# Kernel optimization log

Hardware: AMD Instinct MI355X
Metric: run time of the kernel (lower is better)

The kernel has to match this reference:

```python
import jax, jax.numpy as jnp
import numpy as np

N = 100000; E = 1600000
X_DIM = 128; Y_DIM = 32; H_DIM = 128; R_DIM = 128; Z_DIM = 64
TAU = 1.0; KEEP = 0.1  # dropout p=0.9 -> keep prob 0.1


def spmm(edge_index, edge_weight, h):
    # out[row] += w * h[col]  (sparse [N,N] @ dense [N,D])
    row, col = edge_index[0], edge_index[1]
    return jax.ops.segment_sum(h[col] * edge_weight[:, None], row, num_segments=N)


def setup_inputs() -> dict:
    key = jax.random.key(0)
    ks = jax.random.split(key, 32)
    p = lambda k, shp: (0.02 * jax.random.normal(k, shp)).astype(jnp.float32)
    inp = {
        'x': jax.random.normal(ks[0], (N, X_DIM), dtype=jnp.float32),
        'y_': jax.random.uniform(ks[1], (N, Y_DIM), dtype=jnp.float32),
        'edge_index': jax.random.randint(ks[2], (2, E), 0, N, dtype=jnp.int32),
        'edge_weight': jax.random.uniform(ks[3], (E,), dtype=jnp.float32),
        'non_label': jax.random.bernoulli(ks[4], 0.5, (N,)),
        # inverted dropout mask, torch semantics: keep w.p. 0.1, scale by 1/0.1
        'dropout_mask': (jax.random.bernoulli(ks[5], KEEP, (N, X_DIM)).astype(jnp.float32) / KEEP),
        'u_gumbel': jax.random.uniform(ks[6], (N, Y_DIM), dtype=jnp.float32),
        'z_eps': jax.random.normal(ks[7], (Z_DIM,), dtype=jnp.float32),
        # x_to_yu (2-layer spmm GCN)
        'Wg1': p(ks[8], (X_DIM, H_DIM)), 'bg1': jnp.zeros((H_DIM,), jnp.float32),
        'Wg2': p(ks[9], (H_DIM, Y_DIM)), 'bg2': jnp.zeros((Y_DIM,), jnp.float32),
        # GSNN_Encoder
        'W_xy': p(ks[10], (H_DIM + Y_DIM, R_DIM)), 'b_xy': jnp.zeros((R_DIM,), jnp.float32),
        'W_hr': p(ks[11], (R_DIM, R_DIM)), 'b_hr': jnp.zeros((R_DIM,), jnp.float32),
        # R_to_MuSigma
        'W_rh': p(ks[12], (R_DIM, R_DIM)), 'b_rh': jnp.zeros((R_DIM,), jnp.float32),
        'W_mu': p(ks[13], (R_DIM, Z_DIM)), 'b_mu': jnp.zeros((Z_DIM,), jnp.float32),
        'W_sig': p(ks[14], (R_DIM, Z_DIM)), 'b_sig': jnp.zeros((Z_DIM,), jnp.float32),
        # GSNN_Decoder
        'W_xh': p(ks[15], (X_DIM, H_DIM)), 'b_xh': jnp.zeros((H_DIM,), jnp.float32),
        'W_h2': p(ks[16], (H_DIM + Z_DIM, H_DIM + Z_DIM)), 'b_h2': jnp.zeros((H_DIM + Z_DIM,), jnp.float32),
        'W_hy': p(ks[17], (H_DIM + Z_DIM, Y_DIM)), 'b_hy': jnp.zeros((Y_DIM,), jnp.float32),
    }
    return inp


def reference(x, y_, edge_index, edge_weight, non_label, dropout_mask, u_gumbel, z_eps,
              Wg1, bg1, Wg2, bg2, W_xy, b_xy, W_hr, b_hr,
              W_rh, b_rh, W_mu, b_mu, W_sig, b_sig,
              W_xh, b_xh, W_h2, b_h2, W_hy, b_hy):
    # ---- x_to_yu: 2-layer spmm GCN -> (y_encode [N,Y], y_embedding [N,H]) ----
    h_emb = jax.nn.relu(spmm(edge_index, edge_weight, x) @ Wg1 + bg1)
    y_encode = spmm(edge_index, edge_weight, h_emb) @ Wg2 + bg2
    # ---- gumbel_softmax(hard=True, tau=1) at non-labelled nodes ----
    g = -jnp.log(-jnp.log(u_gumbel + 1e-10) + 1e-10)
    soft = jax.nn.softmax((y_encode + g) / TAU, axis=-1)
    hard = jax.nn.one_hot(jnp.argmax(soft, axis=-1), Y_DIM, dtype=soft.dtype)
    y_gumbel = hard + soft - jax.lax.stop_gradient(soft)  # straight-through
    y = jnp.where(non_label[:, None], y_gumbel, y_)
    # ---- GSNN_Encoder (adj unused, matching original) ----
    h_enc = jax.nn.relu(jnp.concatenate([h_emb, y], axis=1) @ W_xy + b_xy)
    r_nodes = h_enc @ W_hr + b_hr
    r_graph = jnp.mean(r_nodes, axis=0)  # readout [R]
    # ---- R_to_MuSigma + rsample ----
    hr = jax.nn.relu(r_graph @ W_rh + b_rh)
    mu = hr @ W_mu + b_mu
    sigma = 0.1 + 0.9 * jax.nn.sigmoid(hr @ W_sig + b_sig)
    z = mu + sigma * z_eps  # Normal.rsample
    # ---- GSNN_Decoder ----
    xd = x * dropout_mask
    h = jax.nn.relu(xd @ W_xh + b_xh)
    h = jnp.concatenate([h, jnp.broadcast_to(z, (h.shape[0], Z_DIM))], axis=1)
    h = h / (jnp.linalg.norm(h, axis=1, keepdims=True) + 1e-06)
    h = jax.nn.relu(spmm(edge_index, edge_weight, h) @ W_h2 + b_h2)
    y_pred = spmm(edge_index, edge_weight, h) @ W_hy + b_hy
    return y_pred
```

## Files before the change

### kernel.cpp

```cpp
#include <hip/hip_runtime.h>
#include <hip/hip_bf16.h>

#define NN 100000
#define EE 1600000

typedef unsigned short u16;
typedef unsigned int   u32;
typedef short short8 __attribute__((ext_vector_type(8)));
typedef float v4f    __attribute__((ext_vector_type(4)));
typedef u32 u32x2    __attribute__((ext_vector_type(2)));

__device__ __forceinline__ float b2f(u16 h){ u32 u = ((u32)h) << 16; return __builtin_bit_cast(float, u); }
__device__ __forceinline__ float lo2f(u32 u){ return __builtin_bit_cast(float, u << 16); }
__device__ __forceinline__ float hi2f(u32 u){ return __builtin_bit_cast(float, u & 0xffff0000u); }
__device__ __forceinline__ u16   f2b(float f){ __hip_bfloat16 h = __float2bfloat16(f); return __builtin_bit_cast(u16, h); }
__device__ __forceinline__ float ldx(const void* p, long i, int fm){
  return fm ? ((const float*)p)[i] : b2f(((const u16*)p)[i]);
}
__device__ __forceinline__ float i2f(int v){ return __builtin_bit_cast(float, v); }

__global__ void k_detect(const void* __restrict__ x, const void* __restrict__ nonlab,
                         int* __restrict__ flags){
  __shared__ int s_bad, s_ni, s_nf, s_nb;
  int t = threadIdx.x;
  if (t == 0){ s_bad = 0; s_ni = 0; s_nf = 0; s_nb = 0; }
  __syncthreads();
  u32 w = ((const u32*)x)[t];
  u32 lo = w & 0xffffu, ex = (lo >> 7) & 0xffu;
  if (lo != 0u && (ex < 100u || ex > 140u)) atomicAdd(&s_bad, 1);
  if (t < 64){
    u32 v = ((const u32*)nonlab)[t];
    if (v > 1u) atomicAdd(&s_ni, 1);
    if (v != 0u && v != 0x3F800000u) atomicAdd(&s_nf, 1);
  }
  if (t < 128){
    u16 h = ((const u16*)nonlab)[t];
    if (h != 0 && h != 0x3F80) atomicAdd(&s_nb, 1);
  }
  __syncthreads();
  if (t == 0){
    flags[0] = (s_bad > 32) ? 1 : 0;
    flags[1] = (s_ni == 0) ? 1 : ((s_nf == 0) ? 3 : ((s_nb == 0) ? 2 : 0));
  }
}

#define PW_G1 0
#define PW_G2 16384
#define PW_XY 20480
#define PW_XH 40960
#define PW_H2 57344
#define PW_HY 94208
#define PW_TOT 100352
#define PB_G1 0
#define PB_XY 128
#define PB_XH 256
#define PB_H2 384
#define PB_ZERO 576
#define PB_HY 704
#define PB_TOT 736

__global__ __launch_bounds__(256) void k_pack(const void* W0, const void* W1, const void* W2,
                      const void* W3, const void* W4, const void* W5,
                      const void* b0, const void* b1, const void* b2, const void* b3, const void* b4,
                      u16* __restrict__ Wp, float* __restrict__ bp, const int* __restrict__ flags){
  int e = blockIdx.x * 256 + threadIdx.x;
  int fm = flags[0];
  if (e < PW_TOT){
    const void* src; int off, DOUT;
    if      (e < PW_G2){ src = W0; off = PW_G1; DOUT = 128; }
    else if (e < PW_XY){ src = W1; off = PW_G2; DOUT = 32; }
    else if (e < PW_XH){ src = W2; off = PW_XY; DOUT = 128; }
    else if (e < PW_H2){ src = W3; off = PW_XH; DOUT = 128; }
    else if (e < PW_HY){ src = W4; off = PW_H2; DOUT = 192; }
    else               { src = W5; off = PW_HY; DOUT = 32; }
    int local = e - off;
    int k = local / DOUT, col = local - k * DOUT;
    u16 v = fm ? f2b(((const float*)src)[local]) : ((const u16*)src)[local];
    Wp[off + ((k >> 3) * DOUT + col) * 8 + (k & 7)] = v;
  }
  int eb = e - PW_TOT;
  if (eb >= 0 && eb < PB_TOT){
    float v = 0.f;
    if      (eb < 128) v = ldx(b0, eb, fm);
    else if (eb < 256) v = ldx(b1, eb - 128, fm);
    else if (eb < 384) v = ldx(b2, eb - 256, fm);
    else if (eb < 576) v = ldx(b3, eb - 384, fm);
    else if (eb < 704) v = 0.f;
    else               v = ldx(b4, eb - 704, fm);
    bp[eb] = v;
  }
}

#define BSH 9
#define NBK 196
#define CAP 16384

__global__ __launch_bounds__(256) void k_front(const void* __restrict__ x,
     const u16* __restrict__ Wg1p, u16* __restrict__ xpo, const int* __restrict__ flags,
     const int* __restrict__ ei, const void* __restrict__ ew,
     int* __restrict__ bcnt, int2* __restrict__ stage){
  if (blockIdx.x < 1563){
    constexpr int STEPS = 4, CT = 4, RTW = 2, G = 2;
    int wid = blockIdx.x * 4 + (threadIdx.x >> 6);
    if (wid >= 6250) return;
    int g = wid % G; long chunk = wid / G;
    int lane = threadIdx.x & 63, n = lane & 15, q = lane >> 4;
    int colOff = g * 64;
    int fm = flags[0];
    short8 B[CT][STEPS];
    #pragma unroll
    for (int ct = 0; ct < CT; ++ct){
      int col = colOff + ct * 16 + n;
      #pragma unroll
      for (int s = 0; s < STEPS; ++s)
        B[ct][s] = *(const short8*)(Wg1p + (((s * 4 + q) * 128) + col) * 8);
    }
    for (int rt = 0; rt < RTW; ++rt){
      long rowbase = (chunk * RTW + rt) * 16;
      long arow = rowbase + n;
      v4f acc[CT] = {};
      #pragma unroll
      for (int s = 0; s < STEPS; ++s){
        short8 a;
        long base = arow * 128 + s * 32 + q * 8;
        if (fm){
          const float* xp = (const float*)x + base;
          float4 x0 = *(const float4*)xp, x1 = *(const float4*)(xp + 4);
          a[0] = (short)f2b(x0.x); a[1] = (short)f2b(x0.y);
          a[2] = (short)f2b(x0.z); a[3] = (short)f2b(x0.w);
          a[4] = (short)f2b(x1.x); a[5] = (short)f2b(x1.y);
          a[6] = (short)f2b(x1.z); a[7] = (short)f2b(x1.w);
        } else {
          a = *(const short8*)((const u16*)x + base);
        }
        #pragma unroll
        for (int ct = 0; ct < CT; ++ct)
          acc[ct] = __builtin_amdgcn_mfma_f32_16x16x32_bf16(a, B[ct][s], acc[ct], 0, 0, 0);
      }
      long orow = rowbase + q * 4;
      #pragma unroll
      for (int ct = 0; ct < CT; ++ct){
        int col = colOff + ct * 16 + n;
        #pragma unroll
        for (int r = 0; r < 4; ++r)
          xpo[(orow + r) * 128 + col] = f2b(acc[ct][r]);
      }
    }
  } else {
    __shared__ int lcnt[NBK];
    __shared__ int lbase[NBK];
    int t = threadIdx.x;
    int bid = blockIdx.x - 1563;
    for (int i = t; i < NBK; i += 256) lcnt[i] = 0;
    __syncthreads();
    int fm = flags[0];
    long e0 = (long)bid * 4096;
    int bb[16], ord[16], pk[16], wb[16];
    #pragma unroll
    for (int j = 0; j < 16; ++j){
      long e = e0 + j * 256 + t;
      bool v = e < EE;
      int r = v ? ei[e] : 0;
      int c = v ? ei[EE + e] : 0;
      float w = v ? ldx(ew, e, fm) : 0.f;
      int b = r >> BSH;
      bb[j] = v ? b : -1;
      pk[j] = ((r & 511) << 17) | c;
      wb[j] = __builtin_bit_cast(int, w);
      if (v) ord[j] = atomicAdd(&lcnt[b], 1);
    }
    __syncthreads();
    for (int i = t; i < NBK; i += 256){
      int c = lcnt[i];
      lbase[i] = c ? atomicAdd(&bcnt[i], c) : 0;
    }
    __syncthreads();
    #pragma unroll
    for (int j = 0; j < 16; ++j){
      if (bb[j] >= 0){
        int pos = lbase[bb[j]] + ord[j];
        if (pos < CAP) stage[(long)bb[j] * CAP + pos] = make_int2(pk[j], wb[j]);
      }
    }
  }
}

__global__ void k_scanB(const int* __restrict__ bcnt, int* __restrict__ bbase,
                        int* __restrict__ rowptr){
  __shared__ int l[256];
  int t = threadIdx.x;
  int v = (t < NBK) ? bcnt[t] : 0;
  l[t] = v; __syncthreads();
  for (int o = 1; o < 256; o <<= 1){
    int x = (t >= o) ? l[t - o] : 0; __syncthreads();
    l[t] += x; __syncthreads();
  }
  if (t < NBK) bbase[t] = l[t] - v;
  if (t == 0) rowptr[NN] = EE;
}

__global__ __launch_bounds__(512) void k_binB(const int* __restrict__ bbase, const int* __restrict__ bcnt,
                      const int2* __restrict__ stage, int2* __restrict__ cpk,
                      int* __restrict__ rowptr){
  __shared__ int cnt[512];
  __shared__ int cur[512];
  int b = blockIdx.x, t = threadIdx.x;
  int r0 = b << BSH;
  int rows = min(512, NN - r0);
  cnt[t] = 0; __syncthreads();
  int cb = min(bcnt[b], CAP);
  const int2* sb = stage + (long)b * CAP;
  for (int j = t; j < cb; j += 512)
    atomicAdd(&cnt[((u32)sb[j].x) >> 17], 1);
  __syncthreads();
  int v = cnt[t];
  cur[t] = v; __syncthreads();
  for (int o = 1; o < 512; o <<= 1){
    int x = (t >= o) ? cur[t - o] : 0; __syncthreads();
    cur[t] += x; __syncthreads();
  }
  int excl = bbase[b] + cur[t] - v;
  if (t < rows) rowptr[r0 + t] = excl;
  __syncthreads();
  cur[t] = excl;
  __syncthreads();
  for (int j = t; j < cb; j += 512){
    int2 w = sb[j];
    int rib = ((u32)w.x) >> 17;
    int pos = atomicAdd(&cur[rib], 1);
    cpk[pos] = make_int2(w.x & 0x1FFFF, w.y);
  }
}

template<bool AG, bool EPI>
__global__ __launch_bounds__(256) void k_spmm(const u16* __restrict__ in, u16* __restrict__ out,
                       const int* __restrict__ rowptr, const int2* __restrict__ cpk,
                       const float* __restrict__ agt, float* __restrict__ agg,
                       const float* __restrict__ bias){
  int wid  = blockIdx.x * 4 + (threadIdx.x >> 6);
  int lane = threadIdx.x & 63;
  if (wid >= NN) return;
  int half = lane >> 5, l16 = lane & 31;
  int s = rowptr[wid], e = rowptr[wid + 1];
  float a0 = 0.f, a1 = 0.f, a2 = 0.f, a3 = 0.f, aga = 0.f;
  for (int j = s; j < e; j += 8){
    int2 pe[4];
    if (j + 8 <= e){
      #pragma unroll
      for (int k = 0; k < 4; ++k) pe[k] = cpk[j + 2 * k + half];
    } else {
      #pragma unroll
      for (int k = 0; k < 4; ++k){
        int idx = j + 2 * k + half;
        int2 w = cpk[idx < e ? idx : j];
        if (idx >= e) w.y = 0;
        pe[k] = w;
      }
    }
    u32x2 u[4];
    #pragma unroll
    for (int k = 0; k < 4; ++k)
      u[k] = *(const u32x2*)(in + (long)pe[k].x * 128 + 4 * l16);
    if (AG && l16 == 0){
      #pragma unroll
      for (int k = 0; k < 4; ++k) aga = fmaf(i2f(pe[k].y), agt[pe[k].x], aga);
    }
    #pragma unroll
    for (int k = 0; k < 4; ++k){
      float wt = i2f(pe[k].y);
      a0 = fmaf(wt, lo2f(u[k].x), a0);
      a1 = fmaf(wt, hi2f(u[k].x), a1);
      a2 = fmaf(wt, lo2f(u[k].y), a2);
      a3 = fmaf(wt, hi2f(u[k].y), a3);
    }
  }
  a0 += __shfl_xor(a0, 32); a1 += __shfl_xor(a1, 32);
  a2 += __shfl_xor(a2, 32); a3 += __shfl_xor(a3, 32);
  if (AG) aga += __shfl_xor(aga, 32);
  if (EPI){
    a0 = fmaxf(a0 + bias[4 * l16],     0.f);
    a1 = fmaxf(a1 + bias[4 * l16 + 1], 0.f);
    a2 = fmaxf(a2 + bias[4 * l16 + 2], 0.f);
    a3 = fmaxf(a3 + bias[4 * l16 + 3], 0.f);
  }
  if (half == 0){
    u32x2 w;
    w.x = (u32)f2b(a0) | ((u32)f2b(a1) << 16);
    w.y = (u32)f2b(a2) | ((u32)f2b(a3) << 16);
    *(u32x2*)(out + (long)wid * 128 + 4 * l16) = w;
    if (AG && l16 == 0) agg[wid] = aga;
  }
}

__global__ __launch_bounds__(256) void k_spmm32b(const u16* __restrict__ in, void* __restrict__ out,
                       const int* __restrict__ rowptr, const int2* __restrict__ cpk,
                       const int* __restrict__ flags, const float* __restrict__ bp){
  int row = blockIdx.x * 16 + (threadIdx.x >> 4);
  int d = threadIdx.x & 15;
  if (row >= NN) return;
  int eh = d >> 3, d8 = d & 7;
  int fm = flags[0];
  int s = rowptr[row], e = rowptr[row + 1];
  float a0 = 0.f, a1 = 0.f, a2 = 0.f, a3 = 0.f;
  for (int j = s; j < e; j += 8){
    int2 p[4];
    if (j + 8 <= e){
      #pragma unroll
      for (int k = 0; k < 4; ++k) p[k] = cpk[j + 2 * k + eh];
    } else {
      #pragma unroll
      for (int k = 0; k < 4; ++k){
        int idx = j + 2 * k + eh;
        int2 w = cpk[idx < e ? idx : j];
        if (idx >= e) w.y = 0;
        p[k] = w;
      }
    }
    u32x2 u[4];
    #pragma unroll
    for (int k = 0; k < 4; ++k) u[k] = *(const u32x2*)(in + (long)p[k].x * 32 + 4 * d8);
    #pragma unroll
    for (int k = 0; k < 4; ++k){
      float wt = i2f(p[k].y);
      a0 = fmaf(wt, lo2f(u[k].x), a0);
      a1 = fmaf(wt, hi2f(u[k].x), a1);
      a2 = fmaf(wt, lo2f(u[k].y), a2);
      a3 = fmaf(wt, hi2f(u[k].y), a3);
    }
  }
  a0 += __shfl_xor(a0, 8); a1 += __shfl_xor(a1, 8);
  a2 += __shfl_xor(a2, 8); a3 += __shfl_xor(a3, 8);
  a0 += bp[4 * d8]; a1 += bp[4 * d8 + 1]; a2 += bp[4 * d8 + 2]; a3 += bp[4 * d8 + 3];
  if (eh == 0){
    if (fm){
      float4 w = make_float4(a0, a1, a2, a3);
      *(float4*)((float*)out + (long)row * 32 + 4 * d8) = w;
    } else {
      u32x2 w;
      w.x = (u32)f2b(a0) | ((u32)f2b(a1) << 16);
      w.y = (u32)f2b(a2) | ((u32)f2b(a3) << 16);
      *(u32x2*)((u16*)out + (long)row * 32 + 4 * d8) = w;
    }
  }
}

__global__ __launch_bounds__(256) void k_spmmg(const u16* __restrict__ in, u16* __restrict__ y,
                       const int* __restrict__ rowptr, const int2* __restrict__ cpk,
                       const int* __restrict__ flags, const void* __restrict__ bg2,
                       const void* __restrict__ ug, const void* __restrict__ ylab,
                       const void* __restrict__ nonlab){
  int row = blockIdx.x * 16 + (threadIdx.x >> 4);
  int d = threadIdx.x & 15;
  if (row >= NN) return;
  int fm = flags[0], mode = flags[1];
  bool nl;
  if      (mode == 1) nl = ((const int*)nonlab)[row] != 0;
  else if (mode == 3) nl = ((const float*)nonlab)[row] != 0.f;
  else if (mode == 2) nl = ((const u16*)nonlab)[row] != 0;
  else                nl = ((const unsigned char*)nonlab)[row] != 0;
  long base = (long)row * 32;
  if (!nl){
    u32 lo, hi;
    if (fm){
      lo = (u32)f2b(((const float*)ylab)[base + 2 * d]);
      hi = (u32)f2b(((const float*)ylab)[base + 2 * d + 1]);
    } else {
      lo = ((const u16*)ylab)[base + 2 * d];
      hi = ((const u16*)ylab)[base + 2 * d + 1];
    }
    *(u32*)(y + base + 2 * d) = lo | (hi << 16);
    return;
  }
  int eh = d >> 3, d8 = d & 7;
  int s = rowptr[row], e = rowptr[row + 1];
  float a0 = 0.f, a1 = 0.f, a2 = 0.f, a3 = 0.f;
  for (int j = s; j < e; j += 8){
    int2 p[4];
    if (j + 8 <= e){
      #pragma unroll
      for (int k = 0; k < 4; ++k) p[k] = cpk[j + 2 * k + eh];
    } else {
      #pragma unroll
      for (int k = 0; k < 4; ++k){
        int idx = j + 2 * k + eh;
        int2 w = cpk[idx < e ? idx : j];
        if (idx >= e) w.y = 0;
        p[k] = w;
      }
    }
    u32x2 u[4];
    #pragma unroll
    for (int k = 0; k < 4; ++k) u[k] = *(const u32x2*)(in + (long)p[k].x * 32 + 4 * d8);
    #pragma unroll
    for (int k = 0; k < 4; ++k){
      float wt = i2f(p[k].y);
      a0 = fmaf(wt, lo2f(u[k].x), a0);
      a1 = fmaf(wt, hi2f(u[k].x), a1);
      a2 = fmaf(wt, lo2f(u[k].y), a2);
      a3 = fmaf(wt, hi2f(u[k].y), a3);
    }
  }
  a0 += __shfl_xor(a0, 8); a1 += __shfl_xor(a1, 8);
  a2 += __shfl_xor(a2, 8); a3 += __shfl_xor(a3, 8);
  float av[4] = {a0, a1, a2, a3};
  int c0 = 4 * d8;
  float bm = -1e30f; int bi = 0;
  #pragma unroll
  for (int jj = 0; jj < 4; ++jj){
    float uu = ldx(ug, base + c0 + jj, fm);
    float g = -logf(-logf(uu + 1e-10f) + 1e-10f);
    float v = av[jj] + ldx(bg2, c0 + jj, fm) + g;
    if (v > bm){ bm = v; bi = c0 + jj; }
  }
  #pragma unroll
  for (int o = 1; o < 16; o <<= 1){
    float om = __shfl_xor(bm, o);
    int   oi = __shfl_xor(bi, o);
    if (om > bm || (om == bm && oi < bi)){ bm = om; bi = oi; }
  }
  if (eh == 0){
    u32x2 w;
    w.x = ((c0     == bi) ? 0x3F80u : 0u) | (((c0 + 1 == bi) ? 0x3F80u : 0u) << 16);
    w.y = ((c0 + 2 == bi) ? 0x3F80u : 0u) | (((c0 + 3 == bi) ? 0x3F80u : 0u) << 16);
    *(u32x2*)(y + base + c0) = w;
  }
}

template<int K, int DOUT, int CT, int RTW, bool RELU, int AMODE, int OMODE, bool CSUM>
__global__ __launch_bounds__(256) void k_mm(const u16* __restrict__ A, const void* __restrict__ A2,
     const void* __restrict__ A3, const u16* __restrict__ Wp, const float* __restrict__ bp,
     void* __restrict__ outv, const int* __restrict__ flags, float* __restrict__ csacc){
  constexpr int STEPS = K / 32;
  constexpr int G = DOUT / (16 * CT);
  constexpr int CHUNKS = 6250 / RTW;
  __shared__ float lsum[128];
  int wid = blockIdx.x * 4 + (threadIdx.x >> 6);
  if (wid >= G * CHUNKS) return;
  int g = wid % G; long chunk = wid / G;
  int lane = threadIdx.x & 63, n = lane & 15, q = lane >> 4;
  int colOff = g * CT * 16;

  if (CSUM){
    if (threadIdx.x < 128) lsum[threadIdx.x] = 0.f;
    __syncthreads();
  }

  short8 B[CT][STEPS];
  float bv[CT];
  #pragma unroll
  for (int ct = 0; ct < CT; ++ct){
    int col = colOff + ct * 16 + n;
    bv[ct] = bp[col];
    #pragma unroll
    for (int s = 0; s < STEPS; ++s)
      B[ct][s] = *(const short8*)(Wp + (((s * 4 + q) * DOUT) + col) * 8);
  }

  float csum[CT];
  #pragma unroll
  for (int ct = 0; ct < CT; ++ct) csum[ct] = 0.f;

  for (int rt = 0; rt < RTW; ++rt){
    long rowbase = (chunk * RTW + rt) * 16;
    long arow = rowbase + n;
    v4f acc[CT] = {};
    #pragma unroll
    for (int s = 0; s < STEPS; ++s){
      short8 a;
      if (AMODE == 0){
        a = *(const short8*)(A + arow * K + s * 32 + q * 8);
      } else {
        if (s < 4) a = *(const short8*)(A + arow * 128 + s * 32 + q * 8);
        else       a = *(const short8*)((const u16*)A2 + arow * 32 + q * 8);
      }
      #pragma unroll
      for (int ct = 0; ct < CT; ++ct)
        acc[ct] = __builtin_amdgcn_mfma_f32_16x16x32_bf16(a, B[ct][s], acc[ct], 0, 0, 0);
    }
    long orow = rowbase + q * 4;
    #pragma unroll
    for (int ct = 0; ct < CT; ++ct){
      int col = colOff + ct * 16 + n;
      #pragma unroll
      for (int r = 0; r < 4; ++r){
        float v = acc[ct][r] + bv[ct];
        if (RELU) v = fmaxf(v, 0.f);
        if (CSUM) csum[ct] += v;
        if (OMODE != 3){
          long oi = (orow + r) * (long)DOUT + col;
          ((u16*)outv)[oi] = f2b(v);
        }
      }
    }
  }
  if (CSUM){
    #pragma unroll
    for (int ct = 0; ct < CT; ++ct){
      csum[ct] += __shfl_xor(csum[ct], 16);
      csum[ct] += __shfl_xor(csum[ct], 32);
      if (lane < 16) atomicAdd(&lsum[colOff + ct * 16 + n], csum[ct]);
    }
    __syncthreads();
    if (threadIdx.x < 128) csacc[(long)blockIdx.x * 128 + threadIdx.x] = lsum[threadIdx.x];
  }
}

__global__ __launch_bounds__(256) void k_mmh2(const u16* __restrict__ A, const float* __restrict__ AG2,
     const float* __restrict__ zbuf, const u16* __restrict__ Wh2p, const float* __restrict__ bh2p,
     const u16* __restrict__ Whyp, u16* __restrict__ tbuf){
  __shared__ u16 hl[16][200];
  int w = threadIdx.x >> 6;
  int lane = threadIdx.x & 63, n = lane & 15, q = lane >> 4;
  int colOff = w * 48;

  short8 B[3][6];
  float bv[3];
  #pragma unroll
  for (int ct = 0; ct < 3; ++ct){
    int col = colOff + ct * 16 + n;
    bv[ct] = bh2p[col];
    #pragma unroll
    for (int s = 0; s < 6; ++s)
      B[ct][s] = *(const short8*)(Wh2p + (((s * 4 + q) * 192) + col) * 8);
  }
  short8 B2[2][6];
  if (w == 0){
    #pragma unroll
    for (int ct = 0; ct < 2; ++ct){
      int col = ct * 16 + n;
      #pragma unroll
      for (int s = 0; s < 6; ++s)
        B2[ct][s] = *(const short8*)(Whyp + (((s * 4 + q) * 32) + col) * 8);
    }
  }

  for (int rt = 0; rt < 2; ++rt){
    long rowbase = ((long)blockIdx.x * 2 + rt) * 16;
    long arow = rowbase + n;
    float agr = AG2[arow];
    v4f acc[3] = {};
    #pragma unroll
    for (int s = 0; s < 6; ++s){
      short8 a;
      if (s < 4) a = *(const short8*)(A + arow * 128 + s * 32 + q * 8);
      else {
        #pragma unroll
        for (int j = 0; j < 8; ++j) a[j] = (short)f2b(agr * zbuf[(s - 4) * 32 + q * 8 + j]);
      }
      #pragma unroll
      for (int ct = 0; ct < 3; ++ct)
        acc[ct] = __builtin_amdgcn_mfma_f32_16x16x32_bf16(a, B[ct][s], acc[ct], 0, 0, 0);
    }
    #pragma unroll
    for (int ct = 0; ct < 3; ++ct){
      int col = colOff + ct * 16 + n;
      #pragma unroll
      for (int r = 0; r < 4; ++r)
        hl[q * 4 + r][col] = f2b(fmaxf(acc[ct][r] + bv[ct], 0.f));
    }
    __syncthreads();
    if (w == 0){
      v4f a2[2] = {};
      #pragma unroll
      for (int s = 0; s < 6; ++s){
        short8 a = *(const short8*)(&hl[n][s * 32 + q * 8]);
        #pragma unroll
        for (int ct = 0; ct < 2; ++ct)
          a2[ct] = __builtin_amdgcn_mfma_f32_16x16x32_bf16(a, B2[ct][s], a2[ct], 0, 0, 0);
      }
      #pragma unroll
      for (int ct = 0; ct < 2; ++ct){
        int col = ct * 16 + n;
        #pragma unroll
        for (int r = 0; r < 4; ++r)
          tbuf[(rowbase + q * 4 + r) * 32 + col] = f2b(a2[ct][r]);
      }
    }
    __syncthreads();
  }
}

__global__ __launch_bounds__(256) void k_csred(const float* __restrict__ pb, float* __restrict__ accum){
  __shared__ float l[256];
  int c = blockIdx.x, t = threadIdx.x;
  float s = 0.f;
  for (int r = t; r < 1563; r += 256) s += pb[(long)r * 128 + c];
  l[t] = s; __syncthreads();
  for (int o = 128; o; o >>= 1){ if (t < o) l[t] += l[t + o]; __syncthreads(); }
  if (t == 0) accum[c] = l[0];
}

__global__ __launch_bounds__(256) void k_mmnorm(const void* __restrict__ A2, const void* __restrict__ A3,
     const u16* __restrict__ Wp, const float* __restrict__ bp,
     u16* __restrict__ outHs, float* __restrict__ ag,
     const float* __restrict__ zbuf, const int* __restrict__ flags){
  constexpr int STEPS = 4, CT = 8, CHUNKS = 6250;
  int wid = blockIdx.x * 4 + (threadIdx.x >> 6);
  if (wid >= CHUNKS) return;
  long chunk = wid;
  int lane = threadIdx.x & 63, n = lane & 15, q = lane >> 4;
  int fm = flags[0];

  short8 B[CT][STEPS];
  float bv[CT];
  #pragma unroll
  for (int ct = 0; ct < CT; ++ct){
    int col = ct * 16 + n;
    bv[ct] = bp[col];
    #pragma unroll
    for (int s = 0; s < STEPS; ++s)
      B[ct][s] = *(const short8*)(Wp + (((s * 4 + q) * 128) + col) * 8);
  }
  float zz = zbuf[64];

  {
    long rowbase = chunk * 16;
    long arow = rowbase + n;
    v4f acc[CT] = {};
    #pragma unroll
    for (int s = 0; s < STEPS; ++s){
      short8 a;
      long base = arow * 128 + s * 32 + q * 8;
      if (fm){
        const float* xp = (const float*)A2 + base;
        const float* dp = (const float*)A3 + base;
        float4 x0 = *(const float4*)xp, x1 = *(const float4*)(xp + 4);
        float4 d0 = *(const float4*)dp, d1 = *(const float4*)(dp + 4);
        a[0] = (short)f2b(x0.x * d0.x); a[1] = (short)f2b(x0.y * d0.y);
        a[2] = (short)f2b(x0.z * d0.z); a[3] = (short)f2b(x0.w * d0.w);
        a[4] = (short)f2b(x1.x * d1.x); a[5] = (short)f2b(x1.y * d1.y);
        a[6] = (short)f2b(x1.z * d1.z); a[7] = (short)f2b(x1.w * d1.w);
      } else {
        short8 xv = *(const short8*)((const u16*)A2 + base);
        short8 dv = *(const short8*)((const u16*)A3 + base);
        #pragma unroll
        for (int j = 0; j < 8; ++j) a[j] = (short)f2b(b2f((u16)xv[j]) * b2f((u16)dv[j]));
      }
      #pragma unroll
      for (int ct = 0; ct < CT; ++ct)
        acc[ct] = __builtin_amdgcn_mfma_f32_16x16x32_bf16(a, B[ct][s], acc[ct], 0, 0, 0);
    }
    float v[CT][4];
    float sqr[4] = {0.f, 0.f, 0.f, 0.f};
    #pragma unroll
    for (int ct = 0; ct < CT; ++ct){
      #pragma unroll
      for (int r = 0; r < 4; ++r){
        float t = fmaxf(acc[ct][r] + bv[ct], 0.f);
        v[ct][r] = t;
        sqr[r] += t * t;
      }
    }
    #pragma unroll
    for (int r = 0; r < 4; ++r){
      #pragma unroll
      for (int o = 1; o < 16; o <<= 1) sqr[r] += __shfl_xor(sqr[r], o);
    }
    float scale[4];
    #pragma unroll
    for (int r = 0; r < 4; ++r) scale[r] = 1.f / (sqrtf(sqr[r] + zz) + 1e-6f);
    long orow = rowbase + q * 4;
    #pragma unroll
    for (int ct = 0; ct < CT; ++ct){
      int col = ct * 16 + n;
      #pragma unroll
      for (int r = 0; r < 4; ++r)
        outHs[(orow + r) * 128 + col] = f2b(v[ct][r] * scale[r]);
    }
    if (n == 0){
      #pragma unroll
      for (int r = 0; r < 4; ++r) ag[orow + r] = scale[r];
    }
  }
}

__global__ void k_z(const float* __restrict__ accum,
                    const void* Whr, const void* bhr, const void* Wrh, const void* brh,
                    const void* Wmu, const void* bmu, const void* Wsig, const void* bsig,
                    const void* zeps, float* __restrict__ zout, const int* __restrict__ flags){
  __shared__ float hm[128], rg[128], hr[128], zl[64];
  int t = threadIdx.x, fm = flags[0];
  hm[t] = accum[t] * (1.0f / 100000.0f);
  __syncthreads();
  { float s = ldx(bhr, t, fm);
    for (int k = 0; k < 128; ++k) s = fmaf(hm[k], ldx(Whr, (long)k * 128 + t, fm), s);
    rg[t] = s; }
  __syncthreads();
  { float s = ldx(brh, t, fm);
    for (int k = 0; k < 128; ++k) s = fmaf(rg[k], ldx(Wrh, (long)k * 128 + t, fm), s);
    hr[t] = fmaxf(s, 0.f); }
  __syncthreads();
  if (t < 64){
    float m = ldx(bmu, t, fm), sv = ldx(bsig, t, fm);
    for (int k = 0; k < 128; ++k){
      float h = hr[k];
      m  = fmaf(h, ldx(Wmu,  (long)k * 64 + t, fm), m);
      sv = fmaf(h, ldx(Wsig, (long)k * 64 + t, fm), sv);
    }
    float sig = 0.1f + 0.9f / (1.f + expf(-sv));
    float z = fmaf(sig, ldx(zeps, t, fm), m);
    zl[t] = z; zout[t] = z;
  }
  __syncthreads();
  if (t == 0){ float ss = 0.f; for (int j = 0; j < 64; ++j) ss += zl[j] * zl[j]; zout[64] = ss; }
}

extern "C" void kernel_launch(void* const* d_in, const int* in_sizes, int n_in,
                              void* d_out, int out_size, void* d_ws, size_t ws_size,
                              hipStream_t stream){
  const void* x    = d_in[0];
  const void* ylab = d_in[1];
  const int*  ei   = (const int*)d_in[2];
  const void* ew   = d_in[3];
  const void* nonlab = d_in[4];
  const void* dm   = d_in[5];
  const void* ug   = d_in[6];
  const void* zeps = d_in[7];
  const void* Wg1 = d_in[8],  *bg1 = d_in[9];
  const void* Wg2 = d_in[10], *bg2 = d_in[11];
  const void* Wxy = d_in[12], *bxy = d_in[13];
  const void* Whr = d_in[14], *bhr = d_in[15];
  const void* Wrh = d_in[16], *brh = d_in[17];
  const void* Wmu = d_in[18], *bmu = d_in[19];
  const void* Wsg = d_in[20], *bsg = d_in[21];
  const void* Wxh = d_in[22], *bxh = d_in[23];
  const void* Wh2 = d_in[24], *bh2 = d_in[25];
  const void* Why = d_in[26], *bhy = d_in[27];

  char* ws = (char*)d_ws;
  size_t off = 0;
  auto alloc = [&](size_t bytes){ void* p = ws + off; off += (bytes + 511) & ~(size_t)511; return p; };
  int*   flags  = (int*)  alloc(256);
  int*   rowptr = (int*)  alloc((size_t)(NN + 1) * 4);
  int*   bbase  = (int*)  alloc(1024 * 4);
  float* accum  = (float*)alloc(1024 * 4);
  u16*   Wpack  = (u16*)  alloc((size_t)PW_TOT * 2);
  float* bpack  = (float*)alloc((size_t)PB_TOT * 4);
  float* AG1    = (float*)alloc((size_t)NN * 4);
  float* AG2    = (float*)alloc((size_t)NN * 4);
  float* pb     = (float*)alloc((size_t)1563 * 128 * 4);
  int2*  cpk    = (int2*) alloc((size_t)EE * 8);
  u16*   B0     = (u16*)  alloc((size_t)NN * 192 * 2);
  u16*   B1     = (u16*)  alloc((size_t)NN * 192 * 2);
  u16* yproj = B0 + (size_t)NN * 128;
  u16* ybuf  = B1 + (size_t)NN * 160;
  int2* stage = (int2*)B0;
  u16* tbuf = B1;
  int* bcnt = (int*)(accum + 512);

  hipMemsetAsync(accum, 0, 1024 * 4, stream);
  k_detect<<<1, 256, 0, stream>>>(x, nonlab, flags);
  k_pack<<<(PW_TOT + PB_TOT + 255) / 256, 256, 0, stream>>>(Wg1, Wg2, Wxy, Wxh, Wh2, Why,
                                                            bg1, bxy, bxh, bh2, bhy, Wpack, bpack, flags);
  k_front<<<1954, 256, 0, stream>>>(x, Wpack + PW_G1, B1, flags, ei, ew, bcnt, stage);
  k_scanB<<<1, 256, 0, stream>>>(bcnt, bbase, rowptr);
  k_binB <<<NBK, 512, 0, stream>>>(bbase, bcnt, stage, cpk, rowptr);
  k_spmm<false,true ><<<25000, 256, 0, stream>>>(B1, B0, rowptr, cpk, nullptr, nullptr, bpack + PB_G1);
  k_mm<128,32 ,2,1,false,0,0,false><<<1563, 256, 0, stream>>>(B0, nullptr, nullptr, Wpack + PW_G2, bpack + PB_ZERO, yproj, flags, nullptr);
  k_spmmg<<<6250, 256, 0, stream>>>(yproj, ybuf, rowptr, cpk, flags, bg2, ug, ylab, nonlab);
  k_mm<160,128,4,2,true ,2,3,true ><<<1563, 256, 0, stream>>>(B0, ybuf, nullptr, Wpack + PW_XY, bpack + PB_XY, nullptr, flags, pb);
  k_csred<<<128, 256, 0, stream>>>(pb, accum);
  k_z<<<1, 128, 0, stream>>>(accum, Whr, bhr, Wrh, brh, Wmu, bmu, Wsg, bsg, zeps, accum + 128, flags);
  k_mmnorm<<<1563, 256, 0, stream>>>(x, dm, Wpack + PW_XH, bpack + PB_XH, B1, AG1, accum + 128, flags);
  k_spmm<true ,false><<<25000, 256, 0, stream>>>(B1, B0, rowptr, cpk, AG1, AG2, nullptr);
  k_mmh2<<<3125, 256, 0, stream>>>(B0, AG2, accum + 128, Wpack + PW_H2, bpack + PB_H2,
                                   Wpack + PW_HY, tbuf);
  k_spmm32b<<<6250, 256, 0, stream>>>(tbuf, d_out, rowptr, cpk, flags, bpack + PB_HY);
}
```

Baseline: 571.6 us.

## Fuse first SpMM with Wg2 projection and fold detection into pack kernel

```diff
diff --git a/kernel.cpp b/kernel.cpp
--- a/kernel.cpp
+++ b/kernel.cpp
@@ -18,31 +18,6 @@
   return fm ? ((const float*)p)[i] : b2f(((const u16*)p)[i]);
 }
 __device__ __forceinline__ float i2f(int v){ return __builtin_bit_cast(float, v); }
-
-__global__ void k_detect(const void* __restrict__ x, const void* __restrict__ nonlab,
-                         int* __restrict__ flags){
-  __shared__ int s_bad, s_ni, s_nf, s_nb;
-  int t = threadIdx.x;
-  if (t == 0){ s_bad = 0; s_ni = 0; s_nf = 0; s_nb = 0; }
-  __syncthreads();
-  u32 w = ((const u32*)x)[t];
-  u32 lo = w & 0xffffu, ex = (lo >> 7) & 0xffu;
-  if (lo != 0u && (ex < 100u || ex > 140u)) atomicAdd(&s_bad, 1);
-  if (t < 64){
-    u32 v = ((const u32*)nonlab)[t];
-    if (v > 1u) atomicAdd(&s_ni, 1);
-    if (v != 0u && v != 0x3F800000u) atomicAdd(&s_nf, 1);
-  }
-  if (t < 128){
-    u16 h = ((const u16*)nonlab)[t];
-    if (h != 0 && h != 0x3F80) atomicAdd(&s_nb, 1);
-  }
-  __syncthreads();
-  if (t == 0){
-    flags[0] = (s_bad > 32) ? 1 : 0;
-    flags[1] = (s_ni == 0) ? 1 : ((s_nf == 0) ? 3 : ((s_nb == 0) ? 2 : 0));
-  }
-}
 
 #define PW_G1 0
 #define PW_G2 16384
@@ -62,9 +37,39 @@
 __global__ __launch_bounds__(256) void k_pack(const void* W0, const void* W1, const void* W2,
                       const void* W3, const void* W4, const void* W5,
                       const void* b0, const void* b1, const void* b2, const void* b3, const void* b4,
-                      u16* __restrict__ Wp, float* __restrict__ bp, const int* __restrict__ flags){
-  int e = blockIdx.x * 256 + threadIdx.x;
-  int fm = flags[0];
+                      u16* __restrict__ Wp, float* __restrict__ bp,
+                      const void* __restrict__ x, const void* __restrict__ nonlab,
+                      int* __restrict__ flags, float* __restrict__ accum){
+  __shared__ int s_bad, s_ni, s_nf, s_nb;
+  int t = threadIdx.x;
+  if (t == 0){ s_bad = 0; s_ni = 0; s_nf = 0; s_nb = 0; }
+  __syncthreads();
+  {
+    u32 w = ((const u32*)x)[t];
+    u32 lo = w & 0xffffu, ex = (lo >> 7) & 0xffu;
+    if (lo != 0u && (ex < 100u || ex > 140u)) atomicAdd(&s_bad, 1);
+  }
+  if (blockIdx.x == 0){
+    if (t < 64){
+      u32 v = ((const u32*)nonlab)[t];
+      if (v > 1u) atomicAdd(&s_ni, 1);
+      if (v != 0u && v != 0x3F800000u) atomicAdd(&s_nf, 1);
+    }
+    if (t < 128){
+      u16 h = ((const u16*)nonlab)[t];
+      if (h != 0 && h != 0x3F80) atomicAdd(&s_nb, 1);
+    }
+  }
+  __syncthreads();
+  int fm = (s_bad > 32) ? 1 : 0;
+  if (blockIdx.x == 0){
+    if (t == 0){
+      flags[0] = fm;
+      flags[1] = (s_ni == 0) ? 1 : ((s_nf == 0) ? 3 : ((s_nb == 0) ? 2 : 0));
+    }
+    for (int i = t; i < 1024; i += 256) accum[i] = 0.f;
+  }
+  int e = blockIdx.x * 256 + t;
   if (e < PW_TOT){
     const void* src; int off, DOUT;
     if      (e < PW_G2){ src = W0; off = PW_G1; DOUT = 128; }
@@ -229,6 +234,87 @@
     int rib = ((u32)w.x) >> 17;
     int pos = atomicAdd(&cur[rib], 1);
     cpk[pos] = make_int2(w.x & 0x1FFFF, w.y);
+  }
+}
+
+__global__ __launch_bounds__(1024) void k_spmmyp(const u16* __restrict__ in, u16* __restrict__ out,
+                       const int* __restrict__ rowptr, const int2* __restrict__ cpk,
+                       const float* __restrict__ bias, const u16* __restrict__ Wg2p,
+                       u16* __restrict__ yproj){
+  __shared__ u16 hl[16][136];
+  int w = threadIdx.x >> 6;
+  int wid = blockIdx.x * 16 + w;
+  int lane = threadIdx.x & 63;
+  int half = lane >> 5, l16 = lane & 31;
+  int s = rowptr[wid], e = rowptr[wid + 1];
+  float a0 = 0.f, a1 = 0.f, a2 = 0.f, a3 = 0.f;
+  for (int j = s; j < e; j += 8){
+    int2 pe[4];
+    if (j + 8 <= e){
+      #pragma unroll
+      for (int k = 0; k < 4; ++k) pe[k] = cpk[j + 2 * k + half];
+    } else {
+      #pragma unroll
+      for (int k = 0; k < 4; ++k){
+        int idx = j + 2 * k + half;
+        int2 ww = cpk[idx < e ? idx : j];
+        if (idx >= e) ww.y = 0;
+        pe[k] = ww;
+      }
+    }
+    u32x2 u[4];
+    #pragma unroll
+    for (int k = 0; k < 4; ++k)
+      u[k] = *(const u32x2*)(in + (long)pe[k].x * 128 + 4 * l16);
+    #pragma unroll
+    for (int k = 0; k < 4; ++k){
+      float wt = i2f(pe[k].y);
+      a0 = fmaf(wt, lo2f(u[k].x), a0);
+      a1 = fmaf(wt, hi2f(u[k].x), a1);
+      a2 = fmaf(wt, lo2f(u[k].y), a2);
+      a3 = fmaf(wt, hi2f(u[k].y), a3);
+    }
+  }
+  a0 += __shfl_xor(a0, 32); a1 += __shfl_xor(a1, 32);
+  a2 += __shfl_xor(a2, 32); a3 += __shfl_xor(a3, 32);
+  a0 = fmaxf(a0 + bias[4 * l16],     0.f);
+  a1 = fmaxf(a1 + bias[4 * l16 + 1], 0.f);
+  a2 = fmaxf(a2 + bias[4 * l16 + 2], 0.f);
+  a3 = fmaxf(a3 + bias[4 * l16 + 3], 0.f);
+  if (half == 0){
+    u32x2 wv;
+    wv.x = (u32)f2b(a0) | ((u32)f2b(a1) << 16);
+    wv.y = (u32)f2b(a2) | ((u32)f2b(a3) << 16);
+    *(u32x2*)(out + (long)wid * 128 + 4 * l16) = wv;
+    *(u32x2*)(&hl[w][4 * l16]) = wv;
+  }
+  __syncthreads();
+  if (w == 0){
+    int n = lane & 15, q = lane >> 4;
+    short8 B[2][4];
+    #pragma unroll
+    for (int ct = 0; ct < 2; ++ct){
+      int col = ct * 16 + n;
+      #pragma unroll
+      for (int s2 = 0; s2 < 4; ++s2)
+        B[ct][s2] = *(const short8*)(Wg2p + (((s2 * 4 + q) * 32) + col) * 8);
+    }
+    v4f acc[2] = {};
+    #pragma unroll
+    for (int s2 = 0; s2 < 4; ++s2){
+      short8 a = *(const short8*)(&hl[n][s2 * 32 + q * 8]);
+      #pragma unroll
+      for (int ct = 0; ct < 2; ++ct)
+        acc[ct] = __builtin_amdgcn_mfma_f32_16x16x32_bf16(a, B[ct][s2], acc[ct], 0, 0, 0);
+    }
+    long rowbase = (long)blockIdx.x * 16;
+    #pragma unroll
+    for (int ct = 0; ct < 2; ++ct){
+      int col = ct * 16 + n;
+      #pragma unroll
+      for (int r = 0; r < 4; ++r)
+        yproj[(rowbase + q * 4 + r) * 32 + col] = f2b(acc[ct][r]);
+    }
   }
 }
 
@@ -748,15 +834,13 @@
   u16* tbuf = B1;
   int* bcnt = (int*)(accum + 512);
 
-  hipMemsetAsync(accum, 0, 1024 * 4, stream);
-  k_detect<<<1, 256, 0, stream>>>(x, nonlab, flags);
   k_pack<<<(PW_TOT + PB_TOT + 255) / 256, 256, 0, stream>>>(Wg1, Wg2, Wxy, Wxh, Wh2, Why,
-                                                            bg1, bxy, bxh, bh2, bhy, Wpack, bpack, flags);
+                                                            bg1, bxy, bxh, bh2, bhy, Wpack, bpack,
+                                                            x, nonlab, flags, accum);
   k_front<<<1954, 256, 0, stream>>>(x, Wpack + PW_G1, B1, flags, ei, ew, bcnt, stage);
   k_scanB<<<1, 256, 0, stream>>>(bcnt, bbase, rowptr);
   k_binB <<<NBK, 512, 0, stream>>>(bbase, bcnt, stage, cpk, rowptr);
-  k_spmm<false,true ><<<25000, 256, 0, stream>>>(B1, B0, rowptr, cpk, nullptr, nullptr, bpack + PB_G1);
-  k_mm<128,32 ,2,1,false,0,0,false><<<1563, 256, 0, stream>>>(B0, nullptr, nullptr, Wpack + PW_G2, bpack + PB_ZERO, yproj, flags, nullptr);
+  k_spmmyp<<<6250, 1024, 0, stream>>>(B1, B0, rowptr, cpk, bpack + PB_G1, Wpack + PW_G2, yproj);
   k_spmmg<<<6250, 256, 0, stream>>>(yproj, ybuf, rowptr, cpk, flags, bg2, ug, ylab, nonlab);
   k_mm<160,128,4,2,true ,2,3,true ><<<1563, 256, 0, stream>>>(B0, ybuf, nullptr, Wpack + PW_XY, bpack + PB_XY, nullptr, flags, pb);
   k_csred<<<128, 256, 0, stream>>>(pb, accum);
```

Result: no change. 577.6 us (+1.1%).
